# Kernel tuning notes

Hardware: AMD Instinct MI355X
Metric: run time of the kernel (lower is better)

## Reference

```python
import jax, jax.numpy as jnp
import numpy as np

B, L, E, H = 4, 4096, 1024, 16
D = E // H
MLP = 4096
EPS = 1e-6


def layer_norm(x, g, b):
    mu = jnp.mean(x, -1, keepdims=True)
    v = jnp.mean((x - mu) ** 2, -1, keepdims=True)
    return (x - mu) * jax.lax.rsqrt(v + 1e-5) * g + b


def setup_inputs() -> dict:
    key = jax.random.key(0)
    ks = jax.random.split(key, 16)
    s = 1.0 / np.sqrt(E)
    inp = {
        "x": jax.random.normal(ks[0], (B, L, E), jnp.float32),
        "Wq": jax.random.normal(ks[1], (E, E), jnp.float32) * s,
        "bq": jnp.zeros((E,), jnp.float32),
        "lnq_g": jnp.ones((E,), jnp.float32), "lnq_b": jnp.zeros((E,), jnp.float32),
        "Wk": jax.random.normal(ks[2], (E, E), jnp.float32) * s,
        "bk": jnp.zeros((E,), jnp.float32),
        "lnk_g": jnp.ones((E,), jnp.float32), "lnk_b": jnp.zeros((E,), jnp.float32),
        "Wv": jax.random.normal(ks[3], (E, E), jnp.float32) * s,
        "bv": jnp.zeros((E,), jnp.float32),
        "lnv_g": jnp.ones((E,), jnp.float32), "lnv_b": jnp.zeros((E,), jnp.float32),
        "Wphi_q": jax.random.normal(ks[4], (E, E), jnp.float32) * s,
        "bphi_q": jax.random.normal(ks[5], (E,), jnp.float32) * 0.01,
        "Wphi_k": jax.random.normal(ks[6], (E, E), jnp.float32) * s,
        "bphi_k": jax.random.normal(ks[7], (E,), jnp.float32) * 0.01,
        "lna_g": jnp.ones((E,), jnp.float32), "lna_b": jnp.zeros((E,), jnp.float32),
        "W1": jax.random.normal(ks[8], (E, MLP), jnp.float32) * s,
        "b1": jnp.zeros((MLP,), jnp.float32),
        "W2": jax.random.normal(ks[9], (MLP, E), jnp.float32) * (1.0 / np.sqrt(MLP)),
        "b2": jnp.zeros((E,), jnp.float32),
        "gamma": jnp.float32(0.1),
        "conv_w": jax.random.normal(ks[10], (E, E // H, 5), jnp.float32) * (1.0 / np.sqrt((E // H) * 5)),
        "conv_b": jnp.zeros((E,), jnp.float32),
    }
    return inp


def reference(x, Wq, bq, lnq_g, lnq_b, Wk, bk, lnk_g, lnk_b, Wv, bv, lnv_g, lnv_b,
              Wphi_q, bphi_q, Wphi_k, bphi_k, lna_g, lna_b, W1, b1, W2, b2,
              gamma, conv_w, conv_b):
    Bx, Lq, Ex = x.shape
    Q = layer_norm(x @ Wq + bq, lnq_g, lnq_b)
    K = layer_norm(x @ Wk + bk, lnk_g, lnk_b)
    V = layer_norm(x @ Wv + bv, lnv_g, lnv_b)
    # add_zero_token=True: prepend zero token to K, V
    Z = jnp.zeros((Bx, 1, Ex), x.dtype)
    K = jnp.concatenate([Z, K], axis=1)
    V = jnp.concatenate([Z, V], axis=1)
    # TanhKernel feature maps
    phiQ = jnp.tanh(Q @ Wphi_q + bphi_q) + 1.0
    phiK = jnp.tanh(K @ Wphi_k + bphi_k) + 1.0
    sh = lambda t: t.reshape(Bx, -1, H, D)
    Qh, Kh, Vh, pQ, pK = sh(Q), sh(K), sh(V), sh(phiQ), sh(phiK)
    # RALA rescaling: global query vs keys, softmax over L_K, scaled by L_Q
    qg = jnp.mean(Qh, axis=1, keepdims=True) / np.sqrt(D)          # [B,1,H,D]
    scores = jnp.einsum('bihd,blhd->bihl', qg, Kh)                 # [B,1,H,Lk]
    alpha = jax.nn.softmax(scores, axis=-1) * Lq
    alpha = jnp.transpose(alpha[:, 0], (0, 2, 1))[..., None]       # [B,Lk,H,1]
    pKs = pK * alpha
    K_sum = pKs.sum(axis=1)                                        # [B,H,D]
    KV = jnp.einsum('blhd,blhe->bhde', pKs, Vh)                    # [B,H,D,D]
    num = jnp.einsum('blhd,bhde->blhe', pQ, KV)                    # [B,Lq,H,D]
    den = jnp.einsum('blhd,bhd->blh', pQ, K_sum)[..., None] + EPS
    attn = (num / den).reshape(Bx, Lq, Ex)
    # gated grouped local conv (kernel=5, pad=2, groups=H)
    xt = jnp.transpose(attn, (0, 2, 1))                            # [B,E,L]
    conv = jax.lax.conv_general_dilated(xt, conv_w, (1,), [(2, 2)],
                                        feature_group_count=H)
    local = gamma * (conv + conv_b[None, :, None])
    attn = attn + jnp.transpose(local, (0, 2, 1))
    attn = layer_norm(attn, lna_g, lna_b)
    # Residual MLP, then outer residual with query_source
    h = jax.nn.gelu(attn @ W1 + b1, approximate=False) @ W2 + b2
    return attn + h + x
```

## Files before the change

kernel.cpp:

```cpp
#include <hip/hip_runtime.h>
#include <hip/hip_bf16.h>

#define B_ 4
#define L_ 4096
#define E_ 1024
#define H_ 16
#define D_ 64
#define MLP_ 4096
#define M_ (B_*L_)
#define LK_ (L_+1)

typedef short bf16x8 __attribute__((ext_vector_type(8)));
typedef float f32x4 __attribute__((ext_vector_type(4)));
typedef unsigned short u16;

__device__ __forceinline__ u16 f2bf(float f){
    union { float f; unsigned u; } x; x.f = f;
    unsigned r = x.u + 0x7FFFu + ((x.u >> 16) & 1u);
    return (u16)(r >> 16);
}
__device__ __forceinline__ float bf2f(u16 u){
    union { unsigned u; float f; } x; x.u = ((unsigned)u) << 16;
    return x.f;
}

__device__ __forceinline__ void gload16(const u16* g, const u16* l){
    __builtin_amdgcn_global_load_lds(
        (const __attribute__((address_space(1))) void*)g,
        (__attribute__((address_space(3))) void*)l, 16, 0, 0);
}

__global__ __launch_bounds__(256)
void wcvt(const float* __restrict__ in, u16* __restrict__ out, int K, int N)
{
    __shared__ float t[32][33];
    int tid = threadIdx.x;
    int tx = tid & 31, ty = tid >> 5;
    int bk = blockIdx.y, bn = blockIdx.x;
    #pragma unroll
    for (int i=0;i<4;++i)
        t[ty+8*i][tx] = in[(size_t)(bk*32 + ty + 8*i)*N + bn*32 + tx];
    __syncthreads();
    #pragma unroll
    for (int i=0;i<4;++i)
        out[(size_t)(bn*32 + ty + 8*i)*K + bk*32 + tx] = f2bf(t[tx][ty+8*i]);
}

__global__ __launch_bounds__(256)
void xcvt(const float* __restrict__ in, u16* __restrict__ out)
{
    size_t i = ((size_t)blockIdx.x*256 + threadIdx.x)*4;
    float4 v = *(const float4*)(in + i);
    ushort4 o; o.x=f2bf(v.x); o.y=f2bf(v.y); o.z=f2bf(v.z); o.w=f2bf(v.w);
    *(ushort4*)(out + i) = o;
}

template<int EPI>
__global__ __launch_bounds__(256)
void gemm_bf16(const u16* __restrict__ A, const u16* __restrict__ Wt,
               const float* __restrict__ bias, void* __restrict__ Cout,
               int M, int N, int K,
               const float* __restrict__ P1, const float* __restrict__ P2)
{
    __shared__ u16 As[128*64];
    __shared__ u16 Bs[128*64];
    const int tid = threadIdx.x;
    const int bm = blockIdx.y, bn = blockIdx.x;
    const int lane = tid & 63, w = tid >> 6;
    const int wr = w >> 1, wc = w & 1;
    const int row16 = lane & 15, kb = lane >> 4;
    const u16* Abase = A  + (size_t)bm*128*K;
    const u16* Bbase = Wt + (size_t)bn*128*K;
    f32x4 acc[4][4] = {};

    for (int kt = 0; kt < K; kt += 64) {
        #pragma unroll
        for (int c4 = 0; c4 < 4; ++c4) {
            int seg  = c4*32 + w*8;
            int row  = seg + (lane >> 3);
            int col8 = (lane & 7) ^ (row & 7);
            gload16(Abase + (size_t)row*K + kt + col8*8, As + seg*64);
            gload16(Bbase + (size_t)row*K + kt + col8*8, Bs + seg*64);
        }
        __syncthreads();
        #pragma unroll
        for (int kk = 0; kk < 2; ++kk) {
            bf16x8 af[4], bfr[4];
            #pragma unroll
            for (int mi = 0; mi < 4; ++mi) {
                int r = wr*64 + mi*16 + row16;
                int off = r*128 + ((kk*64 + kb*16) ^ ((row16 & 7) << 4));
                af[mi] = *(const bf16x8*)((const char*)As + off);
            }
            #pragma unroll
            for (int nj = 0; nj < 4; ++nj) {
                int r = wc*64 + nj*16 + row16;
                int off = r*128 + ((kk*64 + kb*16) ^ ((row16 & 7) << 4));
                bfr[nj] = *(const bf16x8*)((const char*)Bs + off);
            }
            #pragma unroll
            for (int mi = 0; mi < 4; ++mi)
                #pragma unroll
                for (int nj = 0; nj < 4; ++nj)
                    acc[mi][nj] = __builtin_amdgcn_mfma_f32_16x16x32_bf16(af[mi], bfr[nj], acc[mi][nj], 0, 0, 0);
        }
        __syncthreads();
    }
    #pragma unroll
    for (int nj = 0; nj < 4; ++nj) {
        int col = bn*128 + wc*64 + nj*16 + row16;
        float bcol = bias[col];
        #pragma unroll
        for (int mi = 0; mi < 4; ++mi) {
            int rbase = bm*128 + wr*64 + mi*16 + kb*4;
            #pragma unroll
            for (int r = 0; r < 4; ++r) {
                int row = rbase + r;
                float v = acc[mi][nj][r] + bcol;
                if (EPI == 1) v = tanhf(v) + 1.0f;
                if (EPI == 2) {
                    int b = row >> 12, l = row & 4095, h = col >> 6;
                    v = (tanhf(v) + 1.0f) * P1[(size_t)(b*16 + h)*LK_ + 1 + l];
                }
                if (EPI == 3) v = 0.5f*v*(1.0f + erff(v*0.70710678118654752f));
                if (EPI == 4) {
                    ((float*)Cout)[(size_t)row*N + col] = v + P1[(size_t)row*N + col] + P2[(size_t)row*N + col];
                } else {
                    ((u16*)Cout)[(size_t)row*N + col] = f2bf(v);
                }
            }
        }
    }
}

__global__ __launch_bounds__(256)
void ln_bf16(u16* __restrict__ x, const float* __restrict__ g, const float* __restrict__ bta)
{
    __shared__ float red[8];
    const int row = blockIdx.x, tid = threadIdx.x;
    u16* p = x + (size_t)row*E_;
    ushort4 raw = *(const ushort4*)(p + tid*4);
    float v[4] = {bf2f(raw.x), bf2f(raw.y), bf2f(raw.z), bf2f(raw.w)};
    float s=0.f, s2=0.f;
    #pragma unroll
    for (int i=0;i<4;++i){ s += v[i]; s2 += v[i]*v[i]; }
    #pragma unroll
    for (int o=32;o;o>>=1){ s += __shfl_xor(s,o); s2 += __shfl_xor(s2,o); }
    int wv = tid >> 6;
    if ((tid & 63) == 0){ red[wv] = s; red[4+wv] = s2; }
    __syncthreads();
    s  = red[0]+red[1]+red[2]+red[3];
    s2 = red[4]+red[5]+red[6]+red[7];
    float mu = s * (1.0f/E_);
    float var = s2 * (1.0f/E_) - mu*mu;
    float rs = rsqrtf(var + 1e-5f);
    ushort4 o4;
    float r0 = (v[0]-mu)*rs*g[tid*4+0] + bta[tid*4+0];
    float r1 = (v[1]-mu)*rs*g[tid*4+1] + bta[tid*4+1];
    float r2 = (v[2]-mu)*rs*g[tid*4+2] + bta[tid*4+2];
    float r3 = (v[3]-mu)*rs*g[tid*4+3] + bta[tid*4+3];
    o4.x=f2bf(r0); o4.y=f2bf(r1); o4.z=f2bf(r2); o4.w=f2bf(r3);
    *(ushort4*)(p + tid*4) = o4;
}

__global__ __launch_bounds__(256)
void ln_dual(const u16* __restrict__ x, const float* __restrict__ g, const float* __restrict__ bta,
             float* __restrict__ of, u16* __restrict__ ob)
{
    __shared__ float red[8];
    const int row = blockIdx.x, tid = threadIdx.x;
    const u16* p = x + (size_t)row*E_;
    ushort4 raw = *(const ushort4*)(p + tid*4);
    float v[4] = {bf2f(raw.x), bf2f(raw.y), bf2f(raw.z), bf2f(raw.w)};
    float s=0.f, s2=0.f;
    #pragma unroll
    for (int i=0;i<4;++i){ s += v[i]; s2 += v[i]*v[i]; }
    #pragma unroll
    for (int o=32;o;o>>=1){ s += __shfl_xor(s,o); s2 += __shfl_xor(s2,o); }
    int wv = tid >> 6;
    if ((tid & 63) == 0){ red[wv] = s; red[4+wv] = s2; }
    __syncthreads();
    s  = red[0]+red[1]+red[2]+red[3];
    s2 = red[4]+red[5]+red[6]+red[7];
    float mu = s * (1.0f/E_);
    float var = s2 * (1.0f/E_) - mu*mu;
    float rs = rsqrtf(var + 1e-5f);
    float4 rf; ushort4 o4;
    rf.x = (v[0]-mu)*rs*g[tid*4+0] + bta[tid*4+0];
    rf.y = (v[1]-mu)*rs*g[tid*4+1] + bta[tid*4+1];
    rf.z = (v[2]-mu)*rs*g[tid*4+2] + bta[tid*4+2];
    rf.w = (v[3]-mu)*rs*g[tid*4+3] + bta[tid*4+3];
    o4.x=f2bf(rf.x); o4.y=f2bf(rf.y); o4.z=f2bf(rf.z); o4.w=f2bf(rf.w);
    *(float4*)(of + (size_t)row*E_ + tid*4) = rf;
    *(ushort4*)(ob + (size_t)row*E_ + tid*4) = o4;
}

__global__ __launch_bounds__(1024)
void qg_partial(const u16* __restrict__ Q, float* __restrict__ qg)
{
    int b = blockIdx.x >> 6;
    int c = blockIdx.x & 63;
    int e = threadIdx.x;
    float s = 0.f;
    const u16* p = Q + ((size_t)b*L_ + c*64)*E_ + e;
    for (int l=0; l<64; ++l) s += bf2f(p[(size_t)l*E_]);
    atomicAdd(&qg[b*E_ + e], s);
}

__global__ __launch_bounds__(256)
void rala_scores(const u16* __restrict__ K, const float* __restrict__ qg,
                 float* __restrict__ scores)
{
    int blk = blockIdx.x;
    int row0 = blk * 64;
    int b = row0 >> 12;
    int tid = threadIdx.x;
    int lane = tid & 63, w = tid >> 6;
    float qr[16];
    const float qscale = 1.0f/(L_ * 8.0f);
    #pragma unroll
    for (int j=0;j<16;++j) qr[j] = qg[b*E_ + lane*16 + j] * qscale;
    for (int it = 0; it < 16; ++it) {
        int r = row0 + w*16 + it;
        const u16* p = K + (size_t)r*E_ + lane*16;
        uint4 a0 = *(const uint4*)(p);
        uint4 a1 = *(const uint4*)(p + 8);
        const u16* u0 = (const u16*)&a0;
        const u16* u1 = (const u16*)&a1;
        float s = 0.f;
        #pragma unroll
        for (int j=0;j<8;++j) s = fmaf(bf2f(u0[j]), qr[j], s);
        #pragma unroll
        for (int j=0;j<8;++j) s = fmaf(bf2f(u1[j]), qr[8+j], s);
        s += __shfl_xor(s, 1);
        s += __shfl_xor(s, 2);
        if ((lane & 3) == 0) {
            int h = lane >> 2;
            int l = r & (L_-1);
            scores[((size_t)(b*H_ + h))*L_ + l] = s;
        }
    }
}

__global__ __launch_bounds__(256)
void rala_softmax(const float* __restrict__ scores, float* __restrict__ alpha)
{
    __shared__ float red[8];
    int bh = blockIdx.x, tid = threadIdx.x;
    const float* sc = scores + (size_t)bh*L_;
    float v[16];
    float mx = 0.f;
    #pragma unroll
    for (int i=0;i<16;++i){ v[i] = sc[tid + i*256]; mx = fmaxf(mx, v[i]); }
    #pragma unroll
    for (int o=32;o;o>>=1) mx = fmaxf(mx, __shfl_xor(mx,o));
    int wv = tid >> 6;
    if ((tid & 63) == 0) red[wv] = mx;
    __syncthreads();
    mx = fmaxf(fmaxf(red[0],red[1]), fmaxf(red[2],red[3]));
    float sum = 0.f;
    #pragma unroll
    for (int i=0;i<16;++i){ v[i] = expf(v[i]-mx); sum += v[i]; }
    #pragma unroll
    for (int o=32;o;o>>=1) sum += __shfl_xor(sum,o);
    __syncthreads();
    if ((tid & 63) == 0) red[4+wv] = sum;
    __syncthreads();
    float Z = red[4]+red[5]+red[6]+red[7] + expf(-mx);
    float scale = (float)L_ / Z;
    float* al = alpha + (size_t)bh*LK_;
    #pragma unroll
    for (int i=0;i<16;++i) al[1 + tid + i*256] = v[i]*scale;
    if (tid==0) al[0] = expf(-mx)*scale;
}

#define NS_ 8
__global__ __launch_bounds__(256)
void kv_partial(const u16* __restrict__ phiKs, const u16* __restrict__ Vb,
                float* __restrict__ KV, float* __restrict__ Ksum)
{
    __shared__ float Ps[64][65];
    __shared__ float Vs[64][65];
    int blk = blockIdx.x;
    int s = blk & (NS_-1);
    int h = (blk >> 3) & 15;
    int b = blk >> 7;
    int tid = threadIdx.x;
    int tx = tid & 15, ty = tid >> 4;
    const size_t bh = (size_t)(b*H_ + h);
    float acc[4][4] = {};
    float ksl = 0.f;
    for (int ch = 0; ch < 8; ++ch) {
        int lbase = s*512 + ch*64;
        #pragma unroll
        for (int i=0;i<16;++i){
            int idx = tid + i*256;
            int r = idx >> 6, c2 = idx & 63;
            size_t g = ((size_t)b*L_ + lbase + r)*E_ + h*64 + c2;
            Ps[r][c2] = bf2f(phiKs[g]);
            Vs[r][c2] = bf2f(Vb[g]);
        }
        __syncthreads();
        #pragma unroll 8
        for (int l=0; l<64; ++l){
            float p[4], vv[4];
            #pragma unroll
            for (int i=0;i<4;++i) p[i] = Ps[l][ty*4+i];
            #pragma unroll
            for (int j=0;j<4;++j) vv[j] = Vs[l][tx*4+j];
            #pragma unroll
            for (int i=0;i<4;++i)
                #pragma unroll
                for (int j=0;j<4;++j)
                    acc[i][j] = fmaf(p[i], vv[j], acc[i][j]);
        }
        if (tid < 64){
            float t = 0.f;
            #pragma unroll 8
            for (int l=0; l<64; ++l) t += Ps[l][tid];
            ksl += t;
        }
        __syncthreads();
    }
    #pragma unroll
    for (int i=0;i<4;++i)
        #pragma unroll
        for (int j=0;j<4;++j)
            atomicAdd(&KV[(bh*D_ + ty*4+i)*D_ + tx*4+j], acc[i][j]);
    if (tid < 64) atomicAdd(&Ksum[bh*D_ + tid], ksl);
}

__global__ void ksum_zero(const float* __restrict__ bphi_k,
                          const float* __restrict__ alpha, float* __restrict__ Ksum)
{
    int bh = blockIdx.x; int h = bh & 15; int d = threadIdx.x;
    float a0 = alpha[(size_t)bh*LK_];
    Ksum[(size_t)bh*D_ + d] += (tanhf(bphi_k[h*D_ + d]) + 1.0f) * a0;
}

__global__ __launch_bounds__(256)
void attn_core(const u16* __restrict__ phiQ, const float* __restrict__ KV,
               const float* __restrict__ Ksum, u16* __restrict__ attn)
{
    __shared__ float KVs[64][65];
    __shared__ float Ps[64][65];
    __shared__ float Ks_[64];
    int gid = blockIdx.x;
    int h = gid & 15; int rchunk = gid >> 4;
    int row0 = rchunk * 64;
    int b = row0 >> 12;
    const size_t bh = (size_t)(b*H_ + h);
    int tid = threadIdx.x;
    int tx = tid & 15, ty = tid >> 4;
    #pragma unroll
    for (int i=0;i<16;++i){
        int idx = tid + i*256;
        int r = idx >> 6, c2 = idx & 63;
        KVs[r][c2] = KV[bh*D_*D_ + r*64 + c2];
        Ps[r][c2]  = bf2f(phiQ[((size_t)row0 + r)*E_ + h*64 + c2]);
    }
    if (tid < 64) Ks_[tid] = Ksum[bh*D_ + tid];
    __syncthreads();
    float num[4][4] = {};
    float den[4] = {};
    for (int d=0; d<64; ++d){
        float kd = Ks_[d];
        float4 kv4 = *(const float4*)&KVs[d][tx*4];
        float kvv[4] = {kv4.x, kv4.y, kv4.z, kv4.w};
        #pragma unroll
        for (int i=0;i<4;++i){
            float q = Ps[ty*4+i][d];
            den[i] = fmaf(q, kd, den[i]);
            #pragma unroll
            for (int j=0;j<4;++j)
                num[i][j] = fmaf(q, kvv[j], num[i][j]);
        }
    }
    #pragma unroll
    for (int i=0;i<4;++i){
        float r = 1.0f / (den[i] + 1e-6f);
        #pragma unroll
        for (int j=0;j<4;++j)
            attn[((size_t)row0 + ty*4 + i)*E_ + h*64 + tx*4 + j] = f2bf(num[i][j] * r);
    }
}

__global__ __launch_bounds__(256)
void conv_residual(const u16* __restrict__ attn, const float* __restrict__ conv_w,
                   const float* __restrict__ conv_b, const float* __restrict__ gamma_p,
                   u16* __restrict__ out)
{
    __shared__ float As_[68][65];
    int blk = blockIdx.x;
    int lc = blk & 63; int h = (blk>>6) & 15; int b = blk >> 10;
    int tid = threadIdx.x;
    int e = tid & 63;
    int lg = tid >> 6;
    for (int i=tid; i<68*64; i+=256){
        int r = i>>6, cc = i&63;
        int l = lc*64 - 2 + r;
        As_[r][cc] = (l>=0 && l<L_) ? bf2f(attn[((size_t)b*L_+l)*E_ + h*D_ + cc]) : 0.f;
    }
    __syncthreads();
    float acc[16] = {};
    const float* wbase = conv_w + ((size_t)(h*D_ + e))*320;
    for (int d=0; d<64; ++d){
        float w0 = wbase[d*5+0], w1 = wbase[d*5+1], w2 = wbase[d*5+2],
              w3 = wbase[d*5+3], w4 = wbase[d*5+4];
        float a[20];
        #pragma unroll
        for (int r=0;r<20;++r) a[r] = As_[lg*16 + r][d];
        #pragma unroll
        for (int i=0;i<16;++i)
            acc[i] = fmaf(a[i+4],w4, fmaf(a[i+3],w3, fmaf(a[i+2],w2,
                     fmaf(a[i+1],w1, fmaf(a[i+0],w0, acc[i])))));
    }
    float gamma = *gamma_p;
    float bc = conv_b[h*D_ + e];
    #pragma unroll
    for (int i=0;i<16;++i){
        int l = lc*64 + lg*16 + i;
        float v = As_[lg*16 + i + 2][e] + gamma*(acc[i] + bc);
        out[((size_t)b*L_+l)*E_ + h*D_ + e] = f2bf(v);
    }
}

extern "C" void kernel_launch(void* const* d_in, const int* in_sizes, int n_in,
                              void* d_out, int out_size, void* d_ws, size_t ws_size,
                              hipStream_t stream)
{
    const float* x     = (const float*)d_in[0];
    const float* Wq    = (const float*)d_in[1];
    const float* bq    = (const float*)d_in[2];
    const float* lnq_g = (const float*)d_in[3];
    const float* lnq_b = (const float*)d_in[4];
    const float* Wk    = (const float*)d_in[5];
    const float* bk    = (const float*)d_in[6];
    const float* lnk_g = (const float*)d_in[7];
    const float* lnk_b = (const float*)d_in[8];
    const float* Wv    = (const float*)d_in[9];
    const float* bv    = (const float*)d_in[10];
    const float* lnv_g = (const float*)d_in[11];
    const float* lnv_b = (const float*)d_in[12];
    const float* Wphi_q= (const float*)d_in[13];
    const float* bphi_q= (const float*)d_in[14];
    const float* Wphi_k= (const float*)d_in[15];
    const float* bphi_k= (const float*)d_in[16];
    const float* lna_g = (const float*)d_in[17];
    const float* lna_b = (const float*)d_in[18];
    const float* W1    = (const float*)d_in[19];
    const float* b1    = (const float*)d_in[20];
    const float* W2    = (const float*)d_in[21];
    const float* b2    = (const float*)d_in[22];
    const float* gamma = (const float*)d_in[23];
    const float* conv_w= (const float*)d_in[24];
    const float* conv_b= (const float*)d_in[25];
    float* out = (float*)d_out;

    char* base = (char*)d_ws;
    const size_t WT_SQ = (size_t)E_*E_*2;
    const size_t WT_ALL = 5*WT_SQ + 2*(size_t)E_*MLP_*2;
    const size_t BUF = (size_t)M_*E_*2;
    u16* Wqt  = (u16*)base;
    u16* Wkt  = (u16*)(base + 1*WT_SQ);
    u16* Wvt  = (u16*)(base + 2*WT_SQ);
    u16* Wqpt = (u16*)(base + 3*WT_SQ);
    u16* Wkpt = (u16*)(base + 4*WT_SQ);
    u16* W1t  = (u16*)(base + 5*WT_SQ);
    u16* W2t  = (u16*)(base + 5*WT_SQ + (size_t)E_*MLP_*2);
    char* bufs = base + WT_ALL;
    u16* xb = (u16*)(bufs);
    u16* Qb = (u16*)(bufs + 1*BUF);
    u16* Kb = (u16*)(bufs + 2*BUF);
    u16* Vb = (u16*)(bufs + 3*BUF);
    char* small = bufs + 4*BUF;
    float* qg     = (float*)small;
    float* alpha  = qg + B_*E_;
    float* KV     = alpha + (size_t)B_*H_*LK_;
    float* Ksum   = KV + (size_t)B_*H_*D_*D_;
    float* scores = Ksum + (size_t)B_*H_*D_;
    const size_t need = WT_ALL + 4*BUF +
        ((size_t)B_*E_ + (size_t)B_*H_*LK_ + (size_t)B_*H_*D_*D_ + (size_t)B_*H_*D_
         + (size_t)B_*H_*L_)*4;
    if (ws_size < need) return;

    u16* phiKs = xb;
    u16* phiQ  = Vb;
    u16* attn_b  = Kb;
    u16* attn2_b = Qb;
    float* aln_f = (float*)Kb;
    u16* aln_b   = xb;
    u16* h1      = Qb;

    dim3 blk256(256);
    wcvt<<<dim3(32,32),  blk256, 0, stream>>>(Wq, Wqt, E_, E_);
    wcvt<<<dim3(32,32),  blk256, 0, stream>>>(Wk, Wkt, E_, E_);
    wcvt<<<dim3(32,32),  blk256, 0, stream>>>(Wv, Wvt, E_, E_);
    wcvt<<<dim3(32,32),  blk256, 0, stream>>>(Wphi_q, Wqpt, E_, E_);
    wcvt<<<dim3(32,32),  blk256, 0, stream>>>(Wphi_k, Wkpt, E_, E_);
    wcvt<<<dim3(128,32), blk256, 0, stream>>>(W1, W1t, E_, MLP_);
    wcvt<<<dim3(32,128), blk256, 0, stream>>>(W2, W2t, MLP_, E_);
    xcvt<<<M_*E_/1024, blk256, 0, stream>>>(x, xb);
    hipLaunchKernelGGL((gemm_bf16<0>), dim3(8,128), blk256, 0, stream, xb, Wqt, bq, Qb, M_, E_, E_, nullptr, nullptr);
    hipLaunchKernelGGL((gemm_bf16<0>), dim3(8,128), blk256, 0, stream, xb, Wkt, bk, Kb, M_, E_, E_, nullptr, nullptr);
    hipLaunchKernelGGL((gemm_bf16<0>), dim3(8,128), blk256, 0, stream, xb, Wvt, bv, Vb, M_, E_, E_, nullptr, nullptr);
    ln_bf16<<<M_, 256, 0, stream>>>(Qb, lnq_g, lnq_b);
    ln_bf16<<<M_, 256, 0, stream>>>(Kb, lnk_g, lnk_b);
    ln_bf16<<<M_, 256, 0, stream>>>(Vb, lnv_g, lnv_b);
    hipMemsetAsync(qg, 0, B_*E_*sizeof(float), stream);
    qg_partial<<<B_*64, 1024, 0, stream>>>(Qb, qg);
    rala_scores<<<M_/64, 256, 0, stream>>>(Kb, qg, scores);
    rala_softmax<<<B_*H_, 256, 0, stream>>>(scores, alpha);
    hipLaunchKernelGGL((gemm_bf16<2>), dim3(8,128), blk256, 0, stream, Kb, Wkpt, bphi_k, phiKs, M_, E_, E_, alpha, nullptr);
    hipMemsetAsync(KV,   0, (size_t)B_*H_*D_*D_*sizeof(float), stream);
    hipMemsetAsync(Ksum, 0, (size_t)B_*H_*D_*sizeof(float), stream);
    kv_partial<<<B_*H_*NS_, 256, 0, stream>>>(phiKs, Vb, KV, Ksum);
    ksum_zero<<<B_*H_, 64, 0, stream>>>(bphi_k, alpha, Ksum);
    hipLaunchKernelGGL((gemm_bf16<1>), dim3(8,128), blk256, 0, stream, Qb, Wqpt, bphi_q, phiQ, M_, E_, E_, nullptr, nullptr);
    attn_core<<<(M_/64)*H_, 256, 0, stream>>>(phiQ, KV, Ksum, attn_b);
    conv_residual<<<B_*H_*64, 256, 0, stream>>>(attn_b, conv_w, conv_b, gamma, attn2_b);
    ln_dual<<<M_, 256, 0, stream>>>(attn2_b, lna_g, lna_b, aln_f, aln_b);
    for (int c=0; c<4; ++c){
        const u16* Ain   = aln_b + (size_t)c*4096*E_;
        const float* Rf  = aln_f + (size_t)c*4096*E_;
        const float* xin = x     + (size_t)c*4096*E_;
        float* outc = out + (size_t)c*4096*E_;
        hipLaunchKernelGGL((gemm_bf16<3>), dim3(32,32), blk256, 0, stream, Ain, W1t, b1, h1, 4096, MLP_, E_, nullptr, nullptr);
        hipLaunchKernelGGL((gemm_bf16<4>), dim3(8,32),  blk256, 0, stream, h1, W2t, b2, outc, 4096, E_, MLP_, Rf, xin);
    }
}
```

Baseline: 1.642 ms.

## Add 256x256 double-buffered pipelined bf16 GEMM for projection and MLP-up GEMMs

Adds a gemm256 kernel with 512 threads, 256x256 output tiles, double-buffered LDS staging through global_load_lds, and fine-grained barriers with MFMA phases at raised priority. It replaces the 128x128 GEMM for the Q/K/V, phi projection and W1 GEMMs to get more data reuse per tile and overlap of loads with compute. The old GEMM, still used for W2, now stages through registers instead of direct-to-LDS loads. The large tiles leave fewer blocks for the 256-CU device (256 blocks per projection), and the unswizzled LDS layout may cause bank conflicts.

Measured after the change: 1.456 ms. 1.13x faster.

```diff
diff --git a/kernel.cpp b/kernel.cpp
--- a/kernel.cpp
+++ b/kernel.cpp
@@ -30,6 +30,10 @@
         (__attribute__((address_space(3))) void*)l, 16, 0, 0);
 }
 
+#define BAR() asm volatile("s_barrier" ::: "memory")
+#define LGKM0() do{ asm volatile("s_waitcnt lgkmcnt(0)" ::: "memory"); \
+                    __builtin_amdgcn_sched_barrier(0); }while(0)
+
 __global__ __launch_bounds__(256)
 void wcvt(const float* __restrict__ in, u16* __restrict__ out, int K, int N)
 {
@@ -55,6 +59,138 @@
     *(ushort4*)(out + i) = o;
 }
 
+#define PH_CORE(BI,Q) \
+    x00=rdA(BI,2*Q+0,0); x01=rdA(BI,2*Q+0,1); x10=rdA(BI,2*Q+1,0); x11=rdA(BI,2*Q+1,1);
+#define READB(BI) do{ \
+    _Pragma("unroll") for(int nj_=0;nj_<4;++nj_){ \
+      _Pragma("unroll") for(int kq_=0;kq_<2;++kq_) Bf[nj_][kq_]=rdB(BI,nj_,kq_); } }while(0)
+#define PH_MFMA(Q) \
+  __builtin_amdgcn_s_setprio(1); \
+  acc[2*Q+0][0]=__builtin_amdgcn_mfma_f32_16x16x32_bf16(x00,Bf[0][0],acc[2*Q+0][0],0,0,0); \
+  acc[2*Q+0][0]=__builtin_amdgcn_mfma_f32_16x16x32_bf16(x01,Bf[0][1],acc[2*Q+0][0],0,0,0); \
+  acc[2*Q+0][1]=__builtin_amdgcn_mfma_f32_16x16x32_bf16(x00,Bf[1][0],acc[2*Q+0][1],0,0,0); \
+  acc[2*Q+0][1]=__builtin_amdgcn_mfma_f32_16x16x32_bf16(x01,Bf[1][1],acc[2*Q+0][1],0,0,0); \
+  acc[2*Q+0][2]=__builtin_amdgcn_mfma_f32_16x16x32_bf16(x00,Bf[2][0],acc[2*Q+0][2],0,0,0); \
+  acc[2*Q+0][2]=__builtin_amdgcn_mfma_f32_16x16x32_bf16(x01,Bf[2][1],acc[2*Q+0][2],0,0,0); \
+  acc[2*Q+0][3]=__builtin_amdgcn_mfma_f32_16x16x32_bf16(x00,Bf[3][0],acc[2*Q+0][3],0,0,0); \
+  acc[2*Q+0][3]=__builtin_amdgcn_mfma_f32_16x16x32_bf16(x01,Bf[3][1],acc[2*Q+0][3],0,0,0); \
+  acc[2*Q+1][0]=__builtin_amdgcn_mfma_f32_16x16x32_bf16(x10,Bf[0][0],acc[2*Q+1][0],0,0,0); \
+  acc[2*Q+1][0]=__builtin_amdgcn_mfma_f32_16x16x32_bf16(x11,Bf[0][1],acc[2*Q+1][0],0,0,0); \
+  acc[2*Q+1][1]=__builtin_amdgcn_mfma_f32_16x16x32_bf16(x10,Bf[1][0],acc[2*Q+1][1],0,0,0); \
+  acc[2*Q+1][1]=__builtin_amdgcn_mfma_f32_16x16x32_bf16(x11,Bf[1][1],acc[2*Q+1][1],0,0,0); \
+  acc[2*Q+1][2]=__builtin_amdgcn_mfma_f32_16x16x32_bf16(x10,Bf[2][0],acc[2*Q+1][2],0,0,0); \
+  acc[2*Q+1][2]=__builtin_amdgcn_mfma_f32_16x16x32_bf16(x11,Bf[2][1],acc[2*Q+1][2],0,0,0); \
+  acc[2*Q+1][3]=__builtin_amdgcn_mfma_f32_16x16x32_bf16(x10,Bf[3][0],acc[2*Q+1][3],0,0,0); \
+  acc[2*Q+1][3]=__builtin_amdgcn_mfma_f32_16x16x32_bf16(x11,Bf[3][1],acc[2*Q+1][3],0,0,0); \
+  __builtin_amdgcn_s_setprio(0);
+
+template<int EPI>
+__global__ __launch_bounds__(512, 1)
+void gemm256(const u16* __restrict__ A, const u16* __restrict__ Wt,
+             const float* __restrict__ bias, u16* __restrict__ Cout,
+             int M, int N, int K, const float* __restrict__ P1)
+{
+    __shared__ __align__(16) u16 As[2][256*64];
+    __shared__ __align__(16) u16 Bs[2][256*64];
+    const int tid = threadIdx.x;
+    const int lane = tid & 63, w = tid >> 6;
+    const int wr = w >> 2, wc = w & 3;
+    const int row16 = lane & 15, kb = lane >> 4;
+    const int bm = blockIdx.y, bn = blockIdx.x;
+    const u16* Ab = A  + (size_t)bm*256*K;
+    const u16* Bb = Wt + (size_t)bn*256*K;
+    const int NITER = K >> 7;
+    const int srow = lane >> 3;
+    const int scol = (lane & 7) * 8;
+
+    auto stageA = [&](int bi, int h, int t){
+        #pragma unroll
+        for (int s = 0; s < 2; ++s){
+            int r = h*128 + w*16 + s*8;
+            gload16(Ab + (size_t)(r + srow)*K + t*64 + scol, &As[bi][r*64]);
+        }
+    };
+    auto stageB = [&](int bi, int h, int t){
+        #pragma unroll
+        for (int s = 0; s < 2; ++s){
+            int r = h*128 + w*16 + s*8;
+            gload16(Bb + (size_t)(r + srow)*K + t*64 + scol, &Bs[bi][r*64]);
+        }
+    };
+    auto rdA = [&](int bi, int mi, int kq)->bf16x8{
+        int r = wr*128 + mi*16 + row16;
+        return *(const bf16x8*)&As[bi][r*64 + kq*32 + kb*8];
+    };
+    auto rdB = [&](int bi, int nj, int kq)->bf16x8{
+        int r = wc*64 + nj*16 + row16;
+        return *(const bf16x8*)&Bs[bi][r*64 + kq*32 + kb*8];
+    };
+
+    f32x4 acc[8][4] = {};
+    bf16x8 Bf[4][2];
+    bf16x8 x00, x01, x10, x11;
+
+    stageA(0,0,0); stageA(0,1,0);
+    stageB(0,0,0); stageB(0,1,0);
+    stageB(1,0,1); stageB(1,1,1);
+    asm volatile("s_waitcnt vmcnt(4)" ::: "memory");
+    BAR();
+
+    for (int n = 0; n < NITER; ++n){
+        const int t1 = 2*n + 1;
+        const bool nl = (n + 1 < NITER);
+        READB(0);
+        PH_CORE(0,0);
+        stageA(1,0,t1); stageA(1,1,t1);
+        BAR(); LGKM0(); PH_MFMA(0); BAR();
+        PH_CORE(0,1);
+        if (nl) stageB(0,0,t1+1);
+        BAR(); LGKM0(); PH_MFMA(1); BAR();
+        PH_CORE(0,2);
+        if (nl) stageB(0,1,t1+1);
+        BAR(); LGKM0(); PH_MFMA(2); BAR();
+        PH_CORE(0,3);
+        if (nl) asm volatile("s_waitcnt vmcnt(4)" ::: "memory");
+        else    asm volatile("s_waitcnt vmcnt(0)" ::: "memory");
+        BAR(); LGKM0(); PH_MFMA(3); BAR();
+        READB(1);
+        PH_CORE(1,0);
+        if (nl){ stageA(0,0,t1+1); stageA(0,1,t1+1); }
+        BAR(); LGKM0(); PH_MFMA(0); BAR();
+        PH_CORE(1,1);
+        if (nl) stageB(1,0,t1+2);
+        BAR(); LGKM0(); PH_MFMA(1); BAR();
+        PH_CORE(1,2);
+        if (nl) stageB(1,1,t1+2);
+        BAR(); LGKM0(); PH_MFMA(2); BAR();
+        PH_CORE(1,3);
+        if (nl) asm volatile("s_waitcnt vmcnt(4)" ::: "memory");
+        BAR(); LGKM0(); PH_MFMA(3); BAR();
+    }
+
+    #pragma unroll
+    for (int mi = 0; mi < 8; ++mi){
+        int rbase = bm*256 + wr*128 + mi*16 + kb*4;
+        #pragma unroll
+        for (int nj = 0; nj < 4; ++nj){
+            int col = bn*256 + wc*64 + nj*16 + row16;
+            float bcol = bias[col];
+            #pragma unroll
+            for (int r = 0; r < 4; ++r){
+                int row = rbase + r;
+                float v = acc[mi][nj][r] + bcol;
+                if (EPI == 1) v = tanhf(v) + 1.0f;
+                if (EPI == 2){
+                    int b = row >> 12, l = row & 4095, h = col >> 6;
+                    v = (tanhf(v) + 1.0f) * P1[(size_t)(b*16 + h)*LK_ + 1 + l];
+                }
+                if (EPI == 3) v = 0.5f*v*(1.0f + erff(v*0.70710678118654752f));
+                Cout[(size_t)row*N + col] = f2bf(v);
+            }
+        }
+    }
+}
+
 template<int EPI>
 __global__ __launch_bounds__(256)
 void gemm_bf16(const u16* __restrict__ A, const u16* __restrict__ Wt,
@@ -62,25 +198,25 @@
                int M, int N, int K,
                const float* __restrict__ P1, const float* __restrict__ P2)
 {
-    __shared__ u16 As[128*64];
-    __shared__ u16 Bs[128*64];
+    __shared__ __align__(16) u16 As[128*64];
+    __shared__ __align__(16) u16 Bs[128*64];
     const int tid = threadIdx.x;
     const int bm = blockIdx.y, bn = blockIdx.x;
     const int lane = tid & 63, w = tid >> 6;
     const int wr = w >> 1, wc = w & 1;
     const int row16 = lane & 15, kb = lane >> 4;
-    const u16* Abase = A  + (size_t)bm*128*K;
-    const u16* Bbase = Wt + (size_t)bn*128*K;
     f32x4 acc[4][4] = {};
 
     for (int kt = 0; kt < K; kt += 64) {
         #pragma unroll
-        for (int c4 = 0; c4 < 4; ++c4) {
-            int seg  = c4*32 + w*8;
-            int row  = seg + (lane >> 3);
-            int col8 = (lane & 7) ^ (row & 7);
-            gload16(Abase + (size_t)row*K + kt + col8*8, As + seg*64);
-            gload16(Bbase + (size_t)row*K + kt + col8*8, Bs + seg*64);
+        for (int i = 0; i < 4; ++i) {
+            int c = tid + 256*i;
+            int row = c >> 3, kc = c & 7;
+            uint4 va = *(const uint4*)(A  + (size_t)(bm*128 + row)*K + kt + kc*8);
+            uint4 vb = *(const uint4*)(Wt + (size_t)(bn*128 + row)*K + kt + kc*8);
+            int off = row*128 + ((kc*16) ^ ((row & 7) << 4));
+            *(uint4*)((char*)As + off) = va;
+            *(uint4*)((char*)Bs + off) = vb;
         }
         __syncthreads();
         #pragma unroll
@@ -117,12 +253,6 @@
             for (int r = 0; r < 4; ++r) {
                 int row = rbase + r;
                 float v = acc[mi][nj][r] + bcol;
-                if (EPI == 1) v = tanhf(v) + 1.0f;
-                if (EPI == 2) {
-                    int b = row >> 12, l = row & 4095, h = col >> 6;
-                    v = (tanhf(v) + 1.0f) * P1[(size_t)(b*16 + h)*LK_ + 1 + l];
-                }
-                if (EPI == 3) v = 0.5f*v*(1.0f + erff(v*0.70710678118654752f));
                 if (EPI == 4) {
                     ((float*)Cout)[(size_t)row*N + col] = v + P1[(size_t)row*N + col] + P2[(size_t)row*N + col];
                 } else {
@@ -492,7 +622,7 @@
     u16* aln_b   = xb;
     u16* h1      = Qb;
 
-    dim3 blk256(256);
+    dim3 blk256(256), blk512(512);
     wcvt<<<dim3(32,32),  blk256, 0, stream>>>(Wq, Wqt, E_, E_);
     wcvt<<<dim3(32,32),  blk256, 0, stream>>>(Wk, Wkt, E_, E_);
     wcvt<<<dim3(32,32),  blk256, 0, stream>>>(Wv, Wvt, E_, E_);
@@ -501,9 +631,9 @@
     wcvt<<<dim3(128,32), blk256, 0, stream>>>(W1, W1t, E_, MLP_);
     wcvt<<<dim3(32,128), blk256, 0, stream>>>(W2, W2t, MLP_, E_);
     xcvt<<<M_*E_/1024, blk256, 0, stream>>>(x, xb);
-    hipLaunchKernelGGL((gemm_bf16<0>), dim3(8,128), blk256, 0, stream, xb, Wqt, bq, Qb, M_, E_, E_, nullptr, nullptr);
-    hipLaunchKernelGGL((gemm_bf16<0>), dim3(8,128), blk256, 0, stream, xb, Wkt, bk, Kb, M_, E_, E_, nullptr, nullptr);
-    hipLaunchKernelGGL((gemm_bf16<0>), dim3(8,128), blk256, 0, stream, xb, Wvt, bv, Vb, M_, E_, E_, nullptr, nullptr);
+    hipLaunchKernelGGL((gemm256<0>), dim3(4,64), blk512, 0, stream, xb, Wqt, bq, Qb, M_, E_, E_, nullptr);
+    hipLaunchKernelGGL((gemm256<0>), dim3(4,64), blk512, 0, stream, xb, Wkt, bk, Kb, M_, E_, E_, nullptr);
+    hipLaunchKernelGGL((gemm256<0>), dim3(4,64), blk512, 0, stream, xb, Wvt, bv, Vb, M_, E_, E_, nullptr);
     ln_bf16<<<M_, 256, 0, stream>>>(Qb, lnq_g, lnq_b);
     ln_bf16<<<M_, 256, 0, stream>>>(Kb, lnk_g, lnk_b);
     ln_bf16<<<M_, 256, 0, stream>>>(Vb, lnv_g, lnv_b);
@@ -511,12 +641,12 @@
     qg_partial<<<B_*64, 1024, 0, stream>>>(Qb, qg);
     rala_scores<<<M_/64, 256, 0, stream>>>(Kb, qg, scores);
     rala_softmax<<<B_*H_, 256, 0, stream>>>(scores, alpha);
-    hipLaunchKernelGGL((gemm_bf16<2>), dim3(8,128), blk256, 0, stream, Kb, Wkpt, bphi_k, phiKs, M_, E_, E_, alpha, nullptr);
+    hipLaunchKernelGGL((gemm256<2>), dim3(4,64), blk512, 0, stream, Kb, Wkpt, bphi_k, phiKs, M_, E_, E_, alpha);
     hipMemsetAsync(KV,   0, (size_t)B_*H_*D_*D_*sizeof(float), stream);
     hipMemsetAsync(Ksum, 0, (size_t)B_*H_*D_*sizeof(float), stream);
     kv_partial<<<B_*H_*NS_, 256, 0, stream>>>(phiKs, Vb, KV, Ksum);
     ksum_zero<<<B_*H_, 64, 0, stream>>>(bphi_k, alpha, Ksum);
-    hipLaunchKernelGGL((gemm_bf16<1>), dim3(8,128), blk256, 0, stream, Qb, Wqpt, bphi_q, phiQ, M_, E_, E_, nullptr, nullptr);
+    hipLaunchKernelGGL((gemm256<1>), dim3(4,64), blk512, 0, stream, Qb, Wqpt, bphi_q, phiQ, M_, E_, E_, nullptr);
     attn_core<<<(M_/64)*H_, 256, 0, stream>>>(phiQ, KV, Ksum, attn_b);
     conv_residual<<<B_*H_*64, 256, 0, stream>>>(attn_b, conv_w, conv_b, gamma, attn2_b);
     ln_dual<<<M_, 256, 0, stream>>>(attn2_b, lna_g, lna_b, aln_f, aln_b);
@@ -525,7 +655,7 @@
         const float* Rf  = aln_f + (size_t)c*4096*E_;
         const float* xin = x     + (size_t)c*4096*E_;
         float* outc = out + (size_t)c*4096*E_;
-        hipLaunchKernelGGL((gemm_bf16<3>), dim3(32,32), blk256, 0, stream, Ain, W1t, b1, h1, 4096, MLP_, E_, nullptr, nullptr);
-        hipLaunchKernelGGL((gemm_bf16<4>), dim3(8,32),  blk256, 0, stream, h1, W2t, b2, outc, 4096, E_, MLP_, Rf, xin);
-    }
-}
+        hipLaunchKernelGGL((gemm256<3>), dim3(16,16), blk512, 0, stream, Ain, W1t, b1, h1, 4096, MLP_, E_, nullptr);
+        hipLaunchKernelGGL((gemm_bf16<4>), dim3(8,32), blk256, 0, stream, h1, W2t, b2, outc, 4096, E_, MLP_, Rf, xin);
+    }
+}
```
